# Kernel tuning notes

Measured on AMD Instinct MI355X. Metric: run time of the kernel, lower is better.

Reference implementation:

```python
import jax, jax.numpy as jnp
import numpy as np

MODES = 64        # lowest-frequency modes (mode_select_method='')
IN_CH = 512       # in_channels = H * E = 8 * 64
OUT_CH = 512      # out_channels


def setup_inputs() -> dict:
    key = jax.random.key(0)
    ks = jax.random.split(key, 5)
    B, Lq, Lkv, H, E = 32, 1024, 1024, 8, 64
    q = jax.random.normal(ks[0], (B, Lq, H, E), jnp.float32)
    k = jax.random.normal(ks[1], (B, Lkv, H, E), jnp.float32)
    v = jax.random.normal(ks[2], (B, Lkv, H, E), jnp.float32)
    scale = 1.0 / (IN_CH * OUT_CH)
    # complex weights stored as real/imag parts: [8, in//8, out//8, modes]
    Wr = scale * jax.random.uniform(ks[3], (8, IN_CH // 8, OUT_CH // 8, MODES), jnp.float32)
    Wi = scale * jax.random.uniform(ks[4], (8, IN_CH // 8, OUT_CH // 8, MODES), jnp.float32)
    return {"q": q, "k": k, "v": v, "Wr": Wr, "Wi": Wi}


def reference(q, k, v, Wr, Wi):
    # FourierCrossAttention forward (activation='tanh', lowest-mode selection).
    B, Lq, H, E = q.shape
    idx_q = jnp.arange(MODES)   # sorted lowest modes of rfft(seq_len_q)
    idx_kv = jnp.arange(MODES)  # sorted lowest modes of rfft(seq_len_kv)

    xq = jnp.transpose(q, (0, 2, 3, 1))  # [B,H,E,Lq]
    xk = jnp.transpose(k, (0, 2, 3, 1))  # [B,H,E,Lkv]

    xq_ft = jnp.fft.rfft(xq, axis=-1)[..., idx_q]    # [B,H,E,Mq] complex64
    xk_ft = jnp.fft.rfft(xk, axis=-1)[..., idx_kv]   # [B,H,E,Mkv]

    # frequency-domain attention (no conjugation, matching torch einsum)
    xqk_ft = jnp.einsum('bhex,bhey->bhxy', xq_ft, xk_ft)
    xqk_ft = jnp.tanh(xqk_ft)  # complex tanh
    xqkv_ft = jnp.einsum('bhxy,bhey->bhex', xqk_ft, xk_ft)

    W = (Wr + 1j * Wi).astype(jnp.complex64)
    xqkvw = jnp.einsum('bhex,heox->bhox', xqkv_ft, W)  # [B,H,O,Mq]

    out_ft = jnp.zeros((B, H, OUT_CH // 8, Lq // 2 + 1), jnp.complex64)
    out_ft = out_ft.at[..., idx_q].set(xqkvw)
    out = jnp.fft.irfft(out_ft / (IN_CH * OUT_CH), n=Lq, axis=-1)  # [B,H,O,Lq]
    return out
```

## Files before the change

kernel.cpp:

```cpp
#include <hip/hip_runtime.h>
#include <math.h>

#define TWO_PI_F 6.28318530717958647692f

static constexpr size_t XQR_ = 0;
static constexpr size_t XQI_ = 1048576;
static constexpr size_t XKR_ = 2097152;
static constexpr size_t XKI_ = 3145728;
static constexpr size_t TR_  = 4194304;
static constexpr size_t TI_  = 5242880;
static constexpr size_t VR_  = 6291456;
static constexpr size_t VI_  = 7340032;
static constexpr size_t WTR_ = 8388608;
static constexpr size_t WTI_ = 10485760;
static constexpr size_t UR_  = XQR_;
static constexpr size_t UI_  = XQI_;

__device__ __forceinline__ float f4c(const float4 v, int i) {
  return (i == 0) ? v.x : (i == 1) ? v.y : (i == 2) ? v.z : v.w;
}

__device__ __forceinline__ void cmac4(float4& ar, float4& ai, float sr, float si,
                                      const float4 br, const float4 bi) {
  ar.x += sr * br.x - si * bi.x;  ai.x += sr * bi.x + si * br.x;
  ar.y += sr * br.y - si * bi.y;  ai.y += sr * bi.y + si * br.y;
  ar.z += sr * br.z - si * bi.z;  ai.z += sr * bi.z + si * br.z;
  ar.w += sr * br.w - si * bi.w;  ai.w += sr * bi.w + si * br.w;
}

#define DMAC4(AR, AI, Q) \
  AR.x += Q.x * cc; AI.x -= Q.x * ss; \
  AR.y += Q.y * cc; AI.y -= Q.y * ss; \
  AR.z += Q.z * cc; AI.z -= Q.z * ss; \
  AR.w += Q.w * cc; AI.w -= Q.w * ss;

#define RMAC4(A, UR, UI) \
  A.x += cc * UR.x - ss * UI.x; \
  A.y += cc * UR.y - ss * UI.y; \
  A.z += cc * UR.z - ss * UI.z; \
  A.w += cc * UR.w - ss * UI.w;

__global__ __launch_bounds__(256) void wtrans_kernel(const float* __restrict__ Wr,
                                                     const float* __restrict__ Wi,
                                                     float* __restrict__ ws) {
  float* Wtr = ws + WTR_;
  float* Wti = ws + WTI_;
  const int h = blockIdx.x >> 6;
  const int tile = blockIdx.x & 63;
  const int t = threadIdx.x;
  __shared__ float lr[64][68], li_[64][68];
  const size_t rbase = (size_t)h * 262144 + (size_t)tile * 64 * 64;
#pragma unroll
  for (int i = 0; i < 4; ++i) {
    int idx = t + i * 256;
    int r = idx >> 4, x4 = idx & 15;
    float4 a = *(const float4*)(Wr + rbase + (size_t)r * 64 + x4 * 4);
    float4 b = *(const float4*)(Wi + rbase + (size_t)r * 64 + x4 * 4);
    *(float4*)(&lr[r][x4 * 4]) = a;
    *(float4*)(&li_[r][x4 * 4]) = b;
  }
  __syncthreads();
  const size_t wbase = (size_t)h * 262144 + (size_t)tile * 64;
#pragma unroll
  for (int i = 0; i < 4; ++i) {
    int idx = t + i * 256;
    int x = idx >> 4, r4 = idx & 15;
    float4 a, b;
    a.x = lr[r4 * 4 + 0][x]; a.y = lr[r4 * 4 + 1][x];
    a.z = lr[r4 * 4 + 2][x]; a.w = lr[r4 * 4 + 3][x];
    b.x = li_[r4 * 4 + 0][x]; b.y = li_[r4 * 4 + 1][x];
    b.z = li_[r4 * 4 + 2][x]; b.w = li_[r4 * 4 + 3][x];
    *(float4*)(Wtr + wbase + (size_t)x * 4096 + r4 * 4) = a;
    *(float4*)(Wti + wbase + (size_t)x * 4096 + r4 * 4) = b;
  }
}

__global__ __launch_bounds__(256) void dft_kernel(const float* __restrict__ q,
                                                  const float* __restrict__ k,
                                                  float* __restrict__ ws) {
  const int bi = blockIdx.x;
  const int tz = bi >> 8;
  const int b = (bi & 255) >> 3;
  const int het = bi & 7;
  const float* src = tz ? k : q;
  float* dstR = ws + (tz ? XKR_ : XQR_);
  float* dstI = ws + (tz ? XKI_ : XQI_);
  const int t = threadIdx.x;
  const int m = t & 63;
  const int heBase = (t >> 6) * 16;

  __shared__ float tile[64][64];

  float4 aR0 = {0,0,0,0}, aR1 = {0,0,0,0}, aR2 = {0,0,0,0}, aR3 = {0,0,0,0};
  float4 aI0 = {0,0,0,0}, aI1 = {0,0,0,0}, aI2 = {0,0,0,0}, aI3 = {0,0,0,0};
  float cd, sd;
  sincosf((float)m * (TWO_PI_F / 1024.0f), &sd, &cd);

  const float* srcB = src + (size_t)b * 524288 + het * 64;
  for (int c = 0; c < 16; ++c) {
    const int l0 = c * 64;
    __syncthreads();
#pragma unroll
    for (int i = 0; i < 4; ++i) {
      int idx = t + i * 256;
      int li = idx >> 4, h4 = idx & 15;
      *(float4*)(&tile[li][h4 * 4]) =
          *(const float4*)(srcB + (size_t)(l0 + li) * 512 + h4 * 4);
    }
    __syncthreads();
    int p0 = (m * l0) & 1023;
    float cc, ss;
    sincosf((float)p0 * (TWO_PI_F / 1024.0f), &ss, &cc);
#pragma unroll 4
    for (int li = 0; li < 64; ++li) {
      const float4* tr = (const float4*)(&tile[li][heBase]);
      float4 q0 = tr[0], q1 = tr[1], q2 = tr[2], q3 = tr[3];
      DMAC4(aR0, aI0, q0)
      DMAC4(aR1, aI1, q1)
      DMAC4(aR2, aI2, q2)
      DMAC4(aR3, aI3, q3)
      float nc = cc * cd - ss * sd;
      ss = cc * sd + ss * cd;
      cc = nc;
    }
  }
  float* oR = dstR + (size_t)b * 32768 + (size_t)m * 512 + het * 64 + heBase;
  float* oI = dstI + (size_t)b * 32768 + (size_t)m * 512 + het * 64 + heBase;
  ((float4*)oR)[0] = aR0; ((float4*)oR)[1] = aR1;
  ((float4*)oR)[2] = aR2; ((float4*)oR)[3] = aR3;
  ((float4*)oI)[0] = aI0; ((float4*)oI)[1] = aI1;
  ((float4*)oI)[2] = aI2; ((float4*)oI)[3] = aI3;
}

__device__ __forceinline__ void ctanh1(float a, float b, float& re, float& im) {
  float aa = fabsf(a);
  if (aa > 12.0f) {
    re = copysignf(1.0f, a);
    im = 0.0f;
    return;
  }
  float e2 = __expf(2.0f * aa);
  float ie = 1.0f / e2;
  float sh = 0.5f * (e2 - ie);
  float ch = 0.5f * (e2 + ie);
  float s2, c2;
  sincosf(2.0f * b, &s2, &c2);
  float d = ch + c2;
  float id = 1.0f / d;
  re = copysignf(sh, a) * id;
  im = s2 * id;
}

__device__ __forceinline__ void ctanh4(const float4 ar, const float4 ai, float4& tr, float4& ti) {
  ctanh1(ar.x, ai.x, tr.x, ti.x);
  ctanh1(ar.y, ai.y, tr.y, ti.y);
  ctanh1(ar.z, ai.z, tr.z, ti.z);
  ctanh1(ar.w, ai.w, tr.w, ti.w);
}

__global__ __launch_bounds__(256) void qk_tanh_kernel(float* __restrict__ ws) {
  const float* XQr = ws + XQR_;
  const float* XQi = ws + XQI_;
  const float* XKr = ws + XKR_;
  const float* XKi = ws + XKI_;
  float* Trp = ws + TR_;
  float* Tip = ws + TI_;
  const int bh = blockIdx.x;
  const int b = bh >> 3, h = bh & 7;
  const int t = threadIdx.x;
  const int x = t >> 2, yg = t & 3;
  __shared__ float Kr[64][68], Ki[64][68];
#pragma unroll
  for (int i = 0; i < 4; ++i) {
    int idx = t + i * 256;
    int yl = idx >> 4, e4 = idx & 15;
    size_t g = (size_t)b * 32768 + (size_t)yl * 512 + h * 64 + e4 * 4;
    float4 vr = *(const float4*)(XKr + g);
    float4 vi = *(const float4*)(XKi + g);
    Kr[e4 * 4 + 0][yl] = vr.x; Kr[e4 * 4 + 1][yl] = vr.y;
    Kr[e4 * 4 + 2][yl] = vr.z; Kr[e4 * 4 + 3][yl] = vr.w;
    Ki[e4 * 4 + 0][yl] = vi.x; Ki[e4 * 4 + 1][yl] = vi.y;
    Ki[e4 * 4 + 2][yl] = vi.z; Ki[e4 * 4 + 3][yl] = vi.w;
  }
  __syncthreads();
  float4 aR0 = {0,0,0,0}, aR1 = {0,0,0,0}, aR2 = {0,0,0,0}, aR3 = {0,0,0,0};
  float4 aI0 = {0,0,0,0}, aI1 = {0,0,0,0}, aI2 = {0,0,0,0}, aI3 = {0,0,0,0};
  const float* qbr = XQr + (size_t)b * 32768 + (size_t)x * 512 + h * 64;
  const float* qbi = XQi + (size_t)b * 32768 + (size_t)x * 512 + h * 64;
  for (int ec = 0; ec < 4; ++ec) {
    float4 pr[4], pim[4];
    const float4* gr = (const float4*)(qbr + ec * 16);
    const float4* gi = (const float4*)(qbi + ec * 16);
    pr[0] = gr[0]; pr[1] = gr[1]; pr[2] = gr[2]; pr[3] = gr[3];
    pim[0] = gi[0]; pim[1] = gi[1]; pim[2] = gi[2]; pim[3] = gi[3];
#pragma unroll
    for (int jj = 0; jj < 16; ++jj) {
      int e = ec * 16 + jj;
      float sr = f4c(pr[jj >> 2], jj & 3);
      float si = f4c(pim[jj >> 2], jj & 3);
      const float4* br = (const float4*)(&Kr[e][yg * 16]);
      const float4* bi = (const float4*)(&Ki[e][yg * 16]);
      cmac4(aR0, aI0, sr, si, br[0], bi[0]);
      cmac4(aR1, aI1, sr, si, br[1], bi[1]);
      cmac4(aR2, aI2, sr, si, br[2], bi[2]);
      cmac4(aR3, aI3, sr, si, br[3], bi[3]);
    }
  }
  float* oR = Trp + ((size_t)bh * 64 + x) * 64 + yg * 16;
  float* oI = Tip + ((size_t)bh * 64 + x) * 64 + yg * 16;
  float4 tR, tI;
  ctanh4(aR0, aI0, tR, tI); ((float4*)oR)[0] = tR; ((float4*)oI)[0] = tI;
  ctanh4(aR1, aI1, tR, tI); ((float4*)oR)[1] = tR; ((float4*)oI)[1] = tI;
  ctanh4(aR2, aI2, tR, tI); ((float4*)oR)[2] = tR; ((float4*)oI)[2] = tI;
  ctanh4(aR3, aI3, tR, tI); ((float4*)oR)[3] = tR; ((float4*)oI)[3] = tI;
}

__global__ __launch_bounds__(256) void xqkv_kernel(float* __restrict__ ws) {
  const float* XKr = ws + XKR_;
  const float* XKi = ws + XKI_;
  const float* Trp = ws + TR_;
  const float* Tip = ws + TI_;
  float* Vr = ws + VR_;
  float* Vi = ws + VI_;
  const int bh = blockIdx.x;
  const int b = bh >> 3, h = bh & 7;
  const int t = threadIdx.x;
  const int x = t >> 2, eg = t & 3;
  __shared__ float Kr[64][64], Ki[64][64];
#pragma unroll
  for (int i = 0; i < 4; ++i) {
    int idx = t + i * 256;
    int yl = idx >> 4, e4 = idx & 15;
    size_t g = (size_t)b * 32768 + (size_t)yl * 512 + h * 64 + e4 * 4;
    *(float4*)(&Kr[yl][e4 * 4]) = *(const float4*)(XKr + g);
    *(float4*)(&Ki[yl][e4 * 4]) = *(const float4*)(XKi + g);
  }
  __syncthreads();
  float4 aR0 = {0,0,0,0}, aR1 = {0,0,0,0}, aR2 = {0,0,0,0}, aR3 = {0,0,0,0};
  float4 aI0 = {0,0,0,0}, aI1 = {0,0,0,0}, aI2 = {0,0,0,0}, aI3 = {0,0,0,0};
  const float* tbr = Trp + ((size_t)bh * 64 + x) * 64;
  const float* tbi = Tip + ((size_t)bh * 64 + x) * 64;
  for (int yc = 0; yc < 4; ++yc) {
    float4 pr[4], pim[4];
    const float4* gr = (const float4*)(tbr + yc * 16);
    const float4* gi = (const float4*)(tbi + yc * 16);
    pr[0] = gr[0]; pr[1] = gr[1]; pr[2] = gr[2]; pr[3] = gr[3];
    pim[0] = gi[0]; pim[1] = gi[1]; pim[2] = gi[2]; pim[3] = gi[3];
#pragma unroll
    for (int jj = 0; jj < 16; ++jj) {
      int y = yc * 16 + jj;
      float sr = f4c(pr[jj >> 2], jj & 3);
      float si = f4c(pim[jj >> 2], jj & 3);
      const float4* br = (const float4*)(&Kr[y][eg * 16]);
      const float4* bi = (const float4*)(&Ki[y][eg * 16]);
      cmac4(aR0, aI0, sr, si, br[0], bi[0]);
      cmac4(aR1, aI1, sr, si, br[1], bi[1]);
      cmac4(aR2, aI2, sr, si, br[2], bi[2]);
      cmac4(aR3, aI3, sr, si, br[3], bi[3]);
    }
  }
  float* oR = Vr + ((size_t)bh * 64 + x) * 64 + eg * 16;
  float* oI = Vi + ((size_t)bh * 64 + x) * 64 + eg * 16;
  ((float4*)oR)[0] = aR0; ((float4*)oR)[1] = aR1;
  ((float4*)oR)[2] = aR2; ((float4*)oR)[3] = aR3;
  ((float4*)oI)[0] = aI0; ((float4*)oI)[1] = aI1;
  ((float4*)oI)[2] = aI2; ((float4*)oI)[3] = aI3;
}

__global__ __launch_bounds__(256) void wmul_kernel(float* __restrict__ ws) {
  const float* Vr = ws + VR_;
  const float* Vi = ws + VI_;
  float* Ur = ws + UR_;
  float* Ui = ws + UI_;
  const float* Wtr = ws + WTR_;
  const float* Wti = ws + WTI_;
  const int h = blockIdx.x >> 6, x = blockIdx.x & 63;
  const int t = threadIdx.x;
  const int bI = t >> 3, og = t & 7;
  __shared__ float Ws_r[64][64], Ws_i[64][64];
  const size_t wb = ((size_t)h * 64 + x) * 4096;
#pragma unroll
  for (int i = 0; i < 4; ++i) {
    int idx = t + i * 256;
    int el = idx >> 4, o4 = idx & 15;
    *(float4*)(&Ws_r[el][o4 * 4]) = *(const float4*)(Wtr + wb + (size_t)el * 64 + o4 * 4);
    *(float4*)(&Ws_i[el][o4 * 4]) = *(const float4*)(Wti + wb + (size_t)el * 64 + o4 * 4);
  }
  __syncthreads();
  float4 aR0 = {0,0,0,0}, aR1 = {0,0,0,0}, aI0 = {0,0,0,0}, aI1 = {0,0,0,0};
  const float* vbr = Vr + (((size_t)bI * 8 + h) * 64 + x) * 64;
  const float* vbi = Vi + (((size_t)bI * 8 + h) * 64 + x) * 64;
  for (int ec = 0; ec < 4; ++ec) {
    float4 pr[4], pim[4];
    const float4* gr = (const float4*)(vbr + ec * 16);
    const float4* gi = (const float4*)(vbi + ec * 16);
    pr[0] = gr[0]; pr[1] = gr[1]; pr[2] = gr[2]; pr[3] = gr[3];
    pim[0] = gi[0]; pim[1] = gi[1]; pim[2] = gi[2]; pim[3] = gi[3];
#pragma unroll
    for (int jj = 0; jj < 16; ++jj) {
      int e = ec * 16 + jj;
      float sr = f4c(pr[jj >> 2], jj & 3);
      float si = f4c(pim[jj >> 2], jj & 3);
      const float4* br = (const float4*)(&Ws_r[e][og * 8]);
      const float4* bi = (const float4*)(&Ws_i[e][og * 8]);
      cmac4(aR0, aI0, sr, si, br[0], bi[0]);
      cmac4(aR1, aI1, sr, si, br[1], bi[1]);
    }
  }
  float* oR = Ur + (((size_t)bI * 8 + h) * 64 + x) * 64 + og * 8;
  float* oI = Ui + (((size_t)bI * 8 + h) * 64 + x) * 64 + og * 8;
  ((float4*)oR)[0] = aR0; ((float4*)oR)[1] = aR1;
  ((float4*)oI)[0] = aI0; ((float4*)oI)[1] = aI1;
}

__global__ __launch_bounds__(256) void idft_kernel(const float* __restrict__ ws,
                                                   float* __restrict__ out) {
  const float* Ur = ws + UR_;
  const float* Ui = ws + UI_;
  const int bh = blockIdx.x >> 4;
  const int lt = blockIdx.x & 15;
  const int t = threadIdx.x;
  const int l = lt * 64 + (t & 63);
  const int og = t >> 6;
  __shared__ float Us_r[64][64], Us_i[64][64];
#pragma unroll
  for (int i = 0; i < 4; ++i) {
    int idx = t + i * 256;
    int ml = idx >> 4, o4 = idx & 15;
    size_t g = ((size_t)bh * 64 + ml) * 64 + o4 * 4;
    *(float4*)(&Us_r[ml][o4 * 4]) = *(const float4*)(Ur + g);
    *(float4*)(&Us_i[ml][o4 * 4]) = *(const float4*)(Ui + g);
  }
  __syncthreads();
  const float4* u0 = (const float4*)(&Us_r[0][og * 16]);
  float4 a0 = u0[0], a1 = u0[1], a2 = u0[2], a3 = u0[3];
  a0.x *= 0.5f; a0.y *= 0.5f; a0.z *= 0.5f; a0.w *= 0.5f;
  a1.x *= 0.5f; a1.y *= 0.5f; a1.z *= 0.5f; a1.w *= 0.5f;
  a2.x *= 0.5f; a2.y *= 0.5f; a2.z *= 0.5f; a2.w *= 0.5f;
  a3.x *= 0.5f; a3.y *= 0.5f; a3.z *= 0.5f; a3.w *= 0.5f;
  float cd, sd;
  sincosf((float)l * (TWO_PI_F / 1024.0f), &sd, &cd);
  float cc = cd, ss = sd;
#pragma unroll 4
  for (int m = 1; m < 64; ++m) {
    const float4* ur = (const float4*)(&Us_r[m][og * 16]);
    const float4* ui = (const float4*)(&Us_i[m][og * 16]);
    float4 r0 = ur[0], r1 = ur[1], r2 = ur[2], r3 = ur[3];
    float4 i0 = ui[0], i1 = ui[1], i2 = ui[2], i3 = ui[3];
    RMAC4(a0, r0, i0)
    RMAC4(a1, r1, i1)
    RMAC4(a2, r2, i2)
    RMAC4(a3, r3, i3)
    float nc = cc * cd - ss * sd;
    ss = cc * sd + ss * cd;
    cc = nc;
  }
  const float SCALE = 7.4505805969238281e-9f;
  float* ob = out + ((size_t)bh * 64 + og * 16) * 1024 + l;
  ob[0 * 1024] = a0.x * SCALE;  ob[1 * 1024] = a0.y * SCALE;
  ob[2 * 1024] = a0.z * SCALE;  ob[3 * 1024] = a0.w * SCALE;
  ob[4 * 1024] = a1.x * SCALE;  ob[5 * 1024] = a1.y * SCALE;
  ob[6 * 1024] = a1.z * SCALE;  ob[7 * 1024] = a1.w * SCALE;
  ob[8 * 1024] = a2.x * SCALE;  ob[9 * 1024] = a2.y * SCALE;
  ob[10 * 1024] = a2.z * SCALE; ob[11 * 1024] = a2.w * SCALE;
  ob[12 * 1024] = a3.x * SCALE; ob[13 * 1024] = a3.y * SCALE;
  ob[14 * 1024] = a3.z * SCALE; ob[15 * 1024] = a3.w * SCALE;
}

extern "C" void kernel_launch(void* const* d_in, const int* in_sizes, int n_in,
                              void* d_out, int out_size, void* d_ws, size_t ws_size,
                              hipStream_t stream) {
  (void)in_sizes; (void)n_in; (void)out_size; (void)ws_size;
  const float* q  = (const float*)d_in[0];
  const float* k  = (const float*)d_in[1];
  const float* Wr = (const float*)d_in[3];
  const float* Wi = (const float*)d_in[4];
  float* out = (float*)d_out;
  float* ws  = (float*)d_ws;

  hipLaunchKernelGGL(wtrans_kernel, dim3(512), dim3(256), 0, stream, Wr, Wi, ws);
  hipLaunchKernelGGL(dft_kernel,    dim3(512), dim3(256), 0, stream, q, k, ws);
  hipLaunchKernelGGL(qk_tanh_kernel,dim3(256), dim3(256), 0, stream, ws);
  hipLaunchKernelGGL(xqkv_kernel,   dim3(256), dim3(256), 0, stream, ws);
  hipLaunchKernelGGL(wmul_kernel,   dim3(512), dim3(256), 0, stream, ws);
  hipLaunchKernelGGL(idft_kernel,   dim3(4096), dim3(256), 0, stream, ws, out);
}
```

Baseline: 421.8 us.

## Rewrite DFT and QK stages in double precision with symmetric folding and retiled kernels

```diff
diff --git a/kernel.cpp b/kernel.cpp
--- a/kernel.cpp
+++ b/kernel.cpp
@@ -1,20 +1,23 @@
 #include <hip/hip_runtime.h>
 #include <math.h>
 
+
+#define TWO_PI_D 6.283185307179586476925286766559
 #define TWO_PI_F 6.28318530717958647692f
 
-static constexpr size_t XQR_ = 0;
-static constexpr size_t XQI_ = 1048576;
-static constexpr size_t XKR_ = 2097152;
-static constexpr size_t XKI_ = 3145728;
-static constexpr size_t TR_  = 4194304;
-static constexpr size_t TI_  = 5242880;
-static constexpr size_t VR_  = 6291456;
-static constexpr size_t VI_  = 7340032;
-static constexpr size_t WTR_ = 8388608;
-static constexpr size_t WTI_ = 10485760;
-static constexpr size_t UR_  = XQR_;
-static constexpr size_t UI_  = XQI_;
+static constexpr size_t MB_ = 1024 * 1024;
+static constexpr size_t XQ64R = 0;
+static constexpr size_t XQ64I = 8 * MB_;
+static constexpr size_t XK64R = 16 * MB_;
+static constexpr size_t XK64I = 24 * MB_;
+static constexpr size_t WTRb  = 0;
+static constexpr size_t WTIb  = 8 * MB_;
+static constexpr size_t TRb   = 32 * MB_;
+static constexpr size_t TIb   = 36 * MB_;
+static constexpr size_t VRb   = 40 * MB_;
+static constexpr size_t VIb   = 44 * MB_;
+static constexpr size_t URb   = 16 * MB_;
+static constexpr size_t UIb   = 20 * MB_;
 
 __device__ __forceinline__ float f4c(const float4 v, int i) {
   return (i == 0) ? v.x : (i == 1) ? v.y : (i == 2) ? v.z : v.w;
@@ -28,23 +31,11 @@
   ar.w += sr * br.w - si * bi.w;  ai.w += sr * bi.w + si * br.w;
 }
 
-#define DMAC4(AR, AI, Q) \
-  AR.x += Q.x * cc; AI.x -= Q.x * ss; \
-  AR.y += Q.y * cc; AI.y -= Q.y * ss; \
-  AR.z += Q.z * cc; AI.z -= Q.z * ss; \
-  AR.w += Q.w * cc; AI.w -= Q.w * ss;
-
-#define RMAC4(A, UR, UI) \
-  A.x += cc * UR.x - ss * UI.x; \
-  A.y += cc * UR.y - ss * UI.y; \
-  A.z += cc * UR.z - ss * UI.z; \
-  A.w += cc * UR.w - ss * UI.w;
-
 __global__ __launch_bounds__(256) void wtrans_kernel(const float* __restrict__ Wr,
                                                      const float* __restrict__ Wi,
-                                                     float* __restrict__ ws) {
-  float* Wtr = ws + WTR_;
-  float* Wti = ws + WTI_;
+                                                     char* __restrict__ wsb) {
+  float* Wtr = (float*)(wsb + WTRb);
+  float* Wti = (float*)(wsb + WTIb);
   const int h = blockIdx.x >> 6;
   const int tile = blockIdx.x & 63;
   const int t = threadIdx.x;
@@ -75,169 +66,208 @@
   }
 }
 
-__global__ __launch_bounds__(256) void dft_kernel(const float* __restrict__ q,
-                                                  const float* __restrict__ k,
-                                                  float* __restrict__ ws) {
+__global__ __launch_bounds__(128) void dft64_kernel(const float* __restrict__ q,
+                                                    const float* __restrict__ k,
+                                                    char* __restrict__ wsb) {
   const int bi = blockIdx.x;
-  const int tz = bi >> 8;
-  const int b = (bi & 255) >> 3;
-  const int het = bi & 7;
+  const int tz = bi >> 9;
+  const int b  = (bi >> 4) & 31;
+  const int het = bi & 15;
   const float* src = tz ? k : q;
-  float* dstR = ws + (tz ? XKR_ : XQR_);
-  float* dstI = ws + (tz ? XKI_ : XQI_);
-  const int t = threadIdx.x;
-  const int m = t & 63;
-  const int heBase = (t >> 6) * 16;
-
-  __shared__ float tile[64][64];
-
-  float4 aR0 = {0,0,0,0}, aR1 = {0,0,0,0}, aR2 = {0,0,0,0}, aR3 = {0,0,0,0};
-  float4 aI0 = {0,0,0,0}, aI1 = {0,0,0,0}, aI2 = {0,0,0,0}, aI3 = {0,0,0,0};
-  float cd, sd;
-  sincosf((float)m * (TWO_PI_F / 1024.0f), &sd, &cd);
-
-  const float* srcB = src + (size_t)b * 524288 + het * 64;
+  double* dR = (double*)(wsb + (tz ? XK64R : XQ64R));
+  double* dI = (double*)(wsb + (tz ? XK64I : XQ64I));
+  const int t = threadIdx.x;
+  const int mt = t & 31;
+  const int heg = t >> 5;
+  const int heL = heg * 8;
+  const int heG = het * 32;
+
+  __shared__ double sA[32][34], dA[32][34];
+
+  double re[2][8], im[2][8];
+  const float* srcB = src + (size_t)b * 524288 + heG;
+#pragma unroll
+  for (int kk = 0; kk < 8; ++kk) {
+    double x0 = (double)srcB[heL + kk];
+    double x5 = (double)srcB[262144 + heL + kk];
+    double ev = (mt & 1) ? (x0 - x5) : (x0 + x5);
+    re[0][kk] = ev; re[1][kk] = ev;
+    im[0][kk] = 0.0; im[1][kk] = 0.0;
+  }
+  double cc[2], ss[2], cd[2], sd[2];
+#pragma unroll
+  for (int mi = 0; mi < 2; ++mi) {
+    double ang = (double)(mt + mi * 32) * (TWO_PI_D / 1024.0);
+    sincos(ang, &sd[mi], &cd[mi]);
+    cc[mi] = cd[mi]; ss[mi] = sd[mi];
+  }
+  const int jrow = t >> 2, part = t & 3;
   for (int c = 0; c < 16; ++c) {
-    const int l0 = c * 64;
     __syncthreads();
-#pragma unroll
-    for (int i = 0; i < 4; ++i) {
-      int idx = t + i * 256;
-      int li = idx >> 4, h4 = idx & 15;
-      *(float4*)(&tile[li][h4 * 4]) =
-          *(const float4*)(srcB + (size_t)(l0 + li) * 512 + h4 * 4);
+    {
+      int l = c * 32 + jrow + 1;
+      const float* fw = srcB + (size_t)l * 512 + part * 8;
+      const float* mw = srcB + (size_t)(1024 - l) * 512 + part * 8;
+      float4 f0 = *(const float4*)(fw);
+      float4 f1 = *(const float4*)(fw + 4);
+      float4 m0 = *(const float4*)(mw);
+      float4 m1 = *(const float4*)(mw + 4);
+      double fv[8] = {f0.x, f0.y, f0.z, f0.w, f1.x, f1.y, f1.z, f1.w};
+      double mv[8] = {m0.x, m0.y, m0.z, m0.w, m1.x, m1.y, m1.z, m1.w};
+      if (l == 512) {
+#pragma unroll
+        for (int kk = 0; kk < 8; ++kk) { fv[kk] = 0.0; mv[kk] = 0.0; }
+      }
+#pragma unroll
+      for (int kk = 0; kk < 8; ++kk) {
+        sA[jrow][part * 8 + kk] = fv[kk] + mv[kk];
+        dA[jrow][part * 8 + kk] = fv[kk] - mv[kk];
+      }
     }
     __syncthreads();
-    int p0 = (m * l0) & 1023;
-    float cc, ss;
-    sincosf((float)p0 * (TWO_PI_F / 1024.0f), &ss, &cc);
 #pragma unroll 4
-    for (int li = 0; li < 64; ++li) {
-      const float4* tr = (const float4*)(&tile[li][heBase]);
-      float4 q0 = tr[0], q1 = tr[1], q2 = tr[2], q3 = tr[3];
-      DMAC4(aR0, aI0, q0)
-      DMAC4(aR1, aI1, q1)
-      DMAC4(aR2, aI2, q2)
-      DMAC4(aR3, aI3, q3)
-      float nc = cc * cd - ss * sd;
-      ss = cc * sd + ss * cd;
-      cc = nc;
-    }
-  }
-  float* oR = dstR + (size_t)b * 32768 + (size_t)m * 512 + het * 64 + heBase;
-  float* oI = dstI + (size_t)b * 32768 + (size_t)m * 512 + het * 64 + heBase;
-  ((float4*)oR)[0] = aR0; ((float4*)oR)[1] = aR1;
-  ((float4*)oR)[2] = aR2; ((float4*)oR)[3] = aR3;
-  ((float4*)oI)[0] = aI0; ((float4*)oI)[1] = aI1;
-  ((float4*)oI)[2] = aI2; ((float4*)oI)[3] = aI3;
-}
-
-__device__ __forceinline__ void ctanh1(float a, float b, float& re, float& im) {
-  float aa = fabsf(a);
-  if (aa > 12.0f) {
-    re = copysignf(1.0f, a);
+    for (int j = 0; j < 32; ++j) {
+      double sv[8], dv[8];
+#pragma unroll
+      for (int kk = 0; kk < 8; ++kk) { sv[kk] = sA[j][heL + kk]; dv[kk] = dA[j][heL + kk]; }
+#pragma unroll
+      for (int mi = 0; mi < 2; ++mi) {
+#pragma unroll
+        for (int kk = 0; kk < 8; ++kk) {
+          re[mi][kk] = fma(sv[kk], cc[mi], re[mi][kk]);
+          im[mi][kk] = fma(-dv[kk], ss[mi], im[mi][kk]);
+        }
+        double nc = cc[mi] * cd[mi] - ss[mi] * sd[mi];
+        ss[mi] = cc[mi] * sd[mi] + ss[mi] * cd[mi];
+        cc[mi] = nc;
+      }
+    }
+  }
+#pragma unroll
+  for (int mi = 0; mi < 2; ++mi) {
+    int m = mt + mi * 32;
+    double* oR = dR + (size_t)b * 32768 + (size_t)m * 512 + heG + heL;
+    double* oI = dI + (size_t)b * 32768 + (size_t)m * 512 + heG + heL;
+#pragma unroll
+    for (int kk = 0; kk < 8; ++kk) { oR[kk] = re[mi][kk]; oI[kk] = im[mi][kk]; }
+  }
+}
+
+__device__ __forceinline__ void ctanh_d(double a, double b, float& re, float& im) {
+  double aa = fabs(a);
+  if (aa > 12.0) {
+    re = (a >= 0.0) ? 1.0f : -1.0f;
     im = 0.0f;
     return;
   }
-  float e2 = __expf(2.0f * aa);
+  float e2 = __expf((float)(2.0 * aa));
   float ie = 1.0f / e2;
   float sh = 0.5f * (e2 - ie);
   float ch = 0.5f * (e2 + ie);
+  double phi = 2.0 * b;
+  double n = rint(phi * (1.0 / TWO_PI_D));
+  float r = (float)fma(-n, TWO_PI_D, phi);
   float s2, c2;
-  sincosf(2.0f * b, &s2, &c2);
+  sincosf(r, &s2, &c2);
   float d = ch + c2;
   float id = 1.0f / d;
-  re = copysignf(sh, a) * id;
+  re = ((a >= 0.0) ? sh : -sh) * id;
   im = s2 * id;
 }
 
-__device__ __forceinline__ void ctanh4(const float4 ar, const float4 ai, float4& tr, float4& ti) {
-  ctanh1(ar.x, ai.x, tr.x, ti.x);
-  ctanh1(ar.y, ai.y, tr.y, ti.y);
-  ctanh1(ar.z, ai.z, tr.z, ti.z);
-  ctanh1(ar.w, ai.w, tr.w, ti.w);
-}
-
-__global__ __launch_bounds__(256) void qk_tanh_kernel(float* __restrict__ ws) {
-  const float* XQr = ws + XQR_;
-  const float* XQi = ws + XQI_;
-  const float* XKr = ws + XKR_;
-  const float* XKi = ws + XKI_;
-  float* Trp = ws + TR_;
-  float* Tip = ws + TI_;
+__global__ __launch_bounds__(256) void qk_tanh_kernel(char* __restrict__ wsb) {
+  const double* Qr = (const double*)(wsb + XQ64R);
+  const double* Qi = (const double*)(wsb + XQ64I);
+  const double* Kr = (const double*)(wsb + XK64R);
+  const double* Ki = (const double*)(wsb + XK64I);
+  float* Trp = (float*)(wsb + TRb);
+  float* Tip = (float*)(wsb + TIb);
   const int bh = blockIdx.x;
   const int b = bh >> 3, h = bh & 7;
   const int t = threadIdx.x;
-  const int x = t >> 2, yg = t & 3;
-  __shared__ float Kr[64][68], Ki[64][68];
+  const int tx = t & 15, ty = t >> 4;
+  __shared__ double Qsr[16][66], Qsi[16][66], Ksr[16][66], Ksi[16][66];
+  double are[4][4] = {}, aim[4][4] = {};
+  const int row = t >> 2, ep = t & 3;
+  for (int ec = 0; ec < 4; ++ec) {
+    __syncthreads();
+    {
+      size_t g = (size_t)b * 32768 + (size_t)row * 512 + h * 64 + ec * 16 + ep * 4;
+      double2 a0, a1;
+      a0 = *(const double2*)(Qr + g); a1 = *(const double2*)(Qr + g + 2);
+      Qsr[ep*4+0][row] = a0.x; Qsr[ep*4+1][row] = a0.y;
+      Qsr[ep*4+2][row] = a1.x; Qsr[ep*4+3][row] = a1.y;
+      a0 = *(const double2*)(Qi + g); a1 = *(const double2*)(Qi + g + 2);
+      Qsi[ep*4+0][row] = a0.x; Qsi[ep*4+1][row] = a0.y;
+      Qsi[ep*4+2][row] = a1.x; Qsi[ep*4+3][row] = a1.y;
+      a0 = *(const double2*)(Kr + g); a1 = *(const double2*)(Kr + g + 2);
+      Ksr[ep*4+0][row] = a0.x; Ksr[ep*4+1][row] = a0.y;
+      Ksr[ep*4+2][row] = a1.x; Ksr[ep*4+3][row] = a1.y;
+      a0 = *(const double2*)(Ki + g); a1 = *(const double2*)(Ki + g + 2);
+      Ksi[ep*4+0][row] = a0.x; Ksi[ep*4+1][row] = a0.y;
+      Ksi[ep*4+2][row] = a1.x; Ksi[ep*4+3][row] = a1.y;
+    }
+    __syncthreads();
+#pragma unroll 4
+    for (int el = 0; el < 16; ++el) {
+      double qr[4], qi2[4], kr[4], ki2[4];
+#pragma unroll
+      for (int u = 0; u < 4; ++u) {
+        qr[u]  = Qsr[el][tx * 4 + u];
+        qi2[u] = Qsi[el][tx * 4 + u];
+        kr[u]  = Ksr[el][ty * 4 + u];
+        ki2[u] = Ksi[el][ty * 4 + u];
+      }
+#pragma unroll
+      for (int xx = 0; xx < 4; ++xx)
+#pragma unroll
+        for (int yy = 0; yy < 4; ++yy) {
+          are[xx][yy] = fma(qr[xx], kr[yy], fma(-qi2[xx], ki2[yy], are[xx][yy]));
+          aim[xx][yy] = fma(qr[xx], ki2[yy], fma(qi2[xx], kr[yy], aim[xx][yy]));
+        }
+    }
+  }
+#pragma unroll
+  for (int xx = 0; xx < 4; ++xx) {
+    int x = tx * 4 + xx;
+    float4 tR, tI;
+    ctanh_d(are[xx][0], aim[xx][0], tR.x, tI.x);
+    ctanh_d(are[xx][1], aim[xx][1], tR.y, tI.y);
+    ctanh_d(are[xx][2], aim[xx][2], tR.z, tI.z);
+    ctanh_d(are[xx][3], aim[xx][3], tR.w, tI.w);
+    *(float4*)(Trp + ((size_t)bh * 64 + x) * 64 + ty * 4) = tR;
+    *(float4*)(Tip + ((size_t)bh * 64 + x) * 64 + ty * 4) = tI;
+  }
+}
+
+__global__ __launch_bounds__(256) void xqkv_kernel(char* __restrict__ wsb) {
+  const double* XKr64 = (const double*)(wsb + XK64R);
+  const double* XKi64 = (const double*)(wsb + XK64I);
+  const float* Trp = (const float*)(wsb + TRb);
+  const float* Tip = (const float*)(wsb + TIb);
+  float* Vr = (float*)(wsb + VRb);
+  float* Vi = (float*)(wsb + VIb);
+  const int bh = blockIdx.x >> 2;
+  const int xt = blockIdx.x & 3;
+  const int b = bh >> 3, h = bh & 7;
+  const int t = threadIdx.x;
+  const int x = xt * 16 + (t >> 4);
+  const int eg = t & 15;
+  __shared__ float Kr[64][64], Ki[64][64];
 #pragma unroll
   for (int i = 0; i < 4; ++i) {
     int idx = t + i * 256;
     int yl = idx >> 4, e4 = idx & 15;
     size_t g = (size_t)b * 32768 + (size_t)yl * 512 + h * 64 + e4 * 4;
-    float4 vr = *(const float4*)(XKr + g);
-    float4 vi = *(const float4*)(XKi + g);
-    Kr[e4 * 4 + 0][yl] = vr.x; Kr[e4 * 4 + 1][yl] = vr.y;
-    Kr[e4 * 4 + 2][yl] = vr.z; Kr[e4 * 4 + 3][yl] = vr.w;
-    Ki[e4 * 4 + 0][yl] = vi.x; Ki[e4 * 4 + 1][yl] = vi.y;
-    Ki[e4 * 4 + 2][yl] = vi.z; Ki[e4 * 4 + 3][yl] = vi.w;
+    double2 r0 = *(const double2*)(XKr64 + g);
+    double2 r1 = *(const double2*)(XKr64 + g + 2);
+    double2 i0 = *(const double2*)(XKi64 + g);
+    double2 i1 = *(const double2*)(XKi64 + g + 2);
+    *(float4*)(&Kr[yl][e4 * 4]) = make_float4((float)r0.x, (float)r0.y, (float)r1.x, (float)r1.y);
+    *(float4*)(&Ki[yl][e4 * 4]) = make_float4((float)i0.x, (float)i0.y, (float)i1.x, (float)i1.y);
   }
   __syncthreads();
-  float4 aR0 = {0,0,0,0}, aR1 = {0,0,0,0}, aR2 = {0,0,0,0}, aR3 = {0,0,0,0};
-  float4 aI0 = {0,0,0,0}, aI1 = {0,0,0,0}, aI2 = {0,0,0,0}, aI3 = {0,0,0,0};
-  const float* qbr = XQr + (size_t)b * 32768 + (size_t)x * 512 + h * 64;
-  const float* qbi = XQi + (size_t)b * 32768 + (size_t)x * 512 + h * 64;
-  for (int ec = 0; ec < 4; ++ec) {
-    float4 pr[4], pim[4];
-    const float4* gr = (const float4*)(qbr + ec * 16);
-    const float4* gi = (const float4*)(qbi + ec * 16);
-    pr[0] = gr[0]; pr[1] = gr[1]; pr[2] = gr[2]; pr[3] = gr[3];
-    pim[0] = gi[0]; pim[1] = gi[1]; pim[2] = gi[2]; pim[3] = gi[3];
-#pragma unroll
-    for (int jj = 0; jj < 16; ++jj) {
-      int e = ec * 16 + jj;
-      float sr = f4c(pr[jj >> 2], jj & 3);
-      float si = f4c(pim[jj >> 2], jj & 3);
-      const float4* br = (const float4*)(&Kr[e][yg * 16]);
-      const float4* bi = (const float4*)(&Ki[e][yg * 16]);
-      cmac4(aR0, aI0, sr, si, br[0], bi[0]);
-      cmac4(aR1, aI1, sr, si, br[1], bi[1]);
-      cmac4(aR2, aI2, sr, si, br[2], bi[2]);
-      cmac4(aR3, aI3, sr, si, br[3], bi[3]);
-    }
-  }
-  float* oR = Trp + ((size_t)bh * 64 + x) * 64 + yg * 16;
-  float* oI = Tip + ((size_t)bh * 64 + x) * 64 + yg * 16;
-  float4 tR, tI;
-  ctanh4(aR0, aI0, tR, tI); ((float4*)oR)[0] = tR; ((float4*)oI)[0] = tI;
-  ctanh4(aR1, aI1, tR, tI); ((float4*)oR)[1] = tR; ((float4*)oI)[1] = tI;
-  ctanh4(aR2, aI2, tR, tI); ((float4*)oR)[2] = tR; ((float4*)oI)[2] = tI;
-  ctanh4(aR3, aI3, tR, tI); ((float4*)oR)[3] = tR; ((float4*)oI)[3] = tI;
-}
-
-__global__ __launch_bounds__(256) void xqkv_kernel(float* __restrict__ ws) {
-  const float* XKr = ws + XKR_;
-  const float* XKi = ws + XKI_;
-  const float* Trp = ws + TR_;
-  const float* Tip = ws + TI_;
-  float* Vr = ws + VR_;
-  float* Vi = ws + VI_;
-  const int bh = blockIdx.x;
-  const int b = bh >> 3, h = bh & 7;
-  const int t = threadIdx.x;
-  const int x = t >> 2, eg = t & 3;
-  __shared__ float Kr[64][64], Ki[64][64];
-#pragma unroll
-  for (int i = 0; i < 4; ++i) {
-    int idx = t + i * 256;
-    int yl = idx >> 4, e4 = idx & 15;
-    size_t g = (size_t)b * 32768 + (size_t)yl * 512 + h * 64 + e4 * 4;
-    *(float4*)(&Kr[yl][e4 * 4]) = *(const float4*)(XKr + g);
-    *(float4*)(&Ki[yl][e4 * 4]) = *(const float4*)(XKi + g);
-  }
-  __syncthreads();
-  float4 aR0 = {0,0,0,0}, aR1 = {0,0,0,0}, aR2 = {0,0,0,0}, aR3 = {0,0,0,0};
-  float4 aI0 = {0,0,0,0}, aI1 = {0,0,0,0}, aI2 = {0,0,0,0}, aI3 = {0,0,0,0};
+  float4 aR = {0,0,0,0}, aI = {0,0,0,0};
   const float* tbr = Trp + ((size_t)bh * 64 + x) * 64;
   const float* tbi = Tip + ((size_t)bh * 64 + x) * 64;
   for (int yc = 0; yc < 4; ++yc) {
@@ -251,32 +281,30 @@
       int y = yc * 16 + jj;
       float sr = f4c(pr[jj >> 2], jj & 3);
       float si = f4c(pim[jj >> 2], jj & 3);
-      const float4* br = (const float4*)(&Kr[y][eg * 16]);
-      const float4* bi = (const float4*)(&Ki[y][eg * 16]);
-      cmac4(aR0, aI0, sr, si, br[0], bi[0]);
-      cmac4(aR1, aI1, sr, si, br[1], bi[1]);
-      cmac4(aR2, aI2, sr, si, br[2], bi[2]);
-      cmac4(aR3, aI3, sr, si, br[3], bi[3]);
-    }
-  }
-  float* oR = Vr + ((size_t)bh * 64 + x) * 64 + eg * 16;
-  float* oI = Vi + ((size_t)bh * 64 + x) * 64 + eg * 16;
-  ((float4*)oR)[0] = aR0; ((float4*)oR)[1] = aR1;
-  ((float4*)oR)[2] = aR2; ((float4*)oR)[3] = aR3;
-  ((float4*)oI)[0] = aI0; ((float4*)oI)[1] = aI1;
-  ((float4*)oI)[2] = aI2; ((float4*)oI)[3] = aI3;
-}
-
-__global__ __launch_bounds__(256) void wmul_kernel(float* __restrict__ ws) {
-  const float* Vr = ws + VR_;
-  const float* Vi = ws + VI_;
-  float* Ur = ws + UR_;
-  float* Ui = ws + UI_;
-  const float* Wtr = ws + WTR_;
-  const float* Wti = ws + WTI_;
-  const int h = blockIdx.x >> 6, x = blockIdx.x & 63;
-  const int t = threadIdx.x;
-  const int bI = t >> 3, og = t & 7;
+      const float4 br = *(const float4*)(&Kr[y][eg * 4]);
+      const float4 bi = *(const float4*)(&Ki[y][eg * 4]);
+      cmac4(aR, aI, sr, si, br, bi);
+    }
+  }
+  float* oR = Vr + ((size_t)bh * 64 + x) * 64 + eg * 4;
+  float* oI = Vi + ((size_t)bh * 64 + x) * 64 + eg * 4;
+  *(float4*)oR = aR;
+  *(float4*)oI = aI;
+}
+
+__global__ __launch_bounds__(256) void wmul_kernel(char* __restrict__ wsb) {
+  const float* Vr = (const float*)(wsb + VRb);
+  const float* Vi = (const float*)(wsb + VIb);
+  float* Ur = (float*)(wsb + URb);
+  float* Ui = (float*)(wsb + UIb);
+  const float* Wtr = (const float*)(wsb + WTRb);
+  const float* Wti = (const float*)(wsb + WTIb);
+  const int h = blockIdx.x >> 7;
+  const int x = (blockIdx.x >> 1) & 63;
+  const int bt = blockIdx.x & 1;
+  const int t = threadIdx.x;
+  const int bI = bt * 16 + (t >> 4);
+  const int og = t & 15;
   __shared__ float Ws_r[64][64], Ws_i[64][64];
   const size_t wb = ((size_t)h * 64 + x) * 4096;
 #pragma unroll
@@ -287,7 +315,7 @@
     *(float4*)(&Ws_i[el][o4 * 4]) = *(const float4*)(Wti + wb + (size_t)el * 64 + o4 * 4);
   }
   __syncthreads();
-  float4 aR0 = {0,0,0,0}, aR1 = {0,0,0,0}, aI0 = {0,0,0,0}, aI1 = {0,0,0,0};
+  float4 aR = {0,0,0,0}, aI = {0,0,0,0};
   const float* vbr = Vr + (((size_t)bI * 8 + h) * 64 + x) * 64;
   const float* vbi = Vi + (((size_t)bI * 8 + h) * 64 + x) * 64;
   for (int ec = 0; ec < 4; ++ec) {
@@ -301,24 +329,23 @@
       int e = ec * 16 + jj;
       float sr = f4c(pr[jj >> 2], jj & 3);
       float si = f4c(pim[jj >> 2], jj & 3);
-      const float4* br = (const float4*)(&Ws_r[e][og * 8]);
-      const float4* bi = (const float4*)(&Ws_i[e][og * 8]);
-      cmac4(aR0, aI0, sr, si, br[0], bi[0]);
-      cmac4(aR1, aI1, sr, si, br[1], bi[1]);
-    }
-  }
-  float* oR = Ur + (((size_t)bI * 8 + h) * 64 + x) * 64 + og * 8;
-  float* oI = Ui + (((size_t)bI * 8 + h) * 64 + x) * 64 + og * 8;
-  ((float4*)oR)[0] = aR0; ((float4*)oR)[1] = aR1;
-  ((float4*)oI)[0] = aI0; ((float4*)oI)[1] = aI1;
-}
-
-__global__ __launch_bounds__(256) void idft_kernel(const float* __restrict__ ws,
+      const float4 br = *(const float4*)(&Ws_r[e][og * 4]);
+      const float4 bi = *(const float4*)(&Ws_i[e][og * 4]);
+      cmac4(aR, aI, sr, si, br, bi);
+    }
+  }
+  float* oR = Ur + (((size_t)bI * 8 + h) * 64 + x) * 64 + og * 4;
+  float* oI = Ui + (((size_t)bI * 8 + h) * 64 + x) * 64 + og * 4;
+  *(float4*)oR = aR;
+  *(float4*)oI = aI;
+}
+
+__global__ __launch_bounds__(256) void idft_kernel(const char* __restrict__ wsb,
                                                    float* __restrict__ out) {
-  const float* Ur = ws + UR_;
-  const float* Ui = ws + UI_;
-  const int bh = blockIdx.x >> 4;
-  const int lt = blockIdx.x & 15;
+  const float* Ur = (const float*)(wsb + URb);
+  const float* Ui = (const float*)(wsb + UIb);
+  const int bh = blockIdx.x >> 2;
+  const int lt = blockIdx.x & 3;
   const int t = threadIdx.x;
   const int l = lt * 64 + (t & 63);
   const int og = t >> 6;
@@ -332,12 +359,14 @@
     *(float4*)(&Us_i[ml][o4 * 4]) = *(const float4*)(Ui + g);
   }
   __syncthreads();
+  float4 a[4][4];
   const float4* u0 = (const float4*)(&Us_r[0][og * 16]);
-  float4 a0 = u0[0], a1 = u0[1], a2 = u0[2], a3 = u0[3];
-  a0.x *= 0.5f; a0.y *= 0.5f; a0.z *= 0.5f; a0.w *= 0.5f;
-  a1.x *= 0.5f; a1.y *= 0.5f; a1.z *= 0.5f; a1.w *= 0.5f;
-  a2.x *= 0.5f; a2.y *= 0.5f; a2.z *= 0.5f; a2.w *= 0.5f;
-  a3.x *= 0.5f; a3.y *= 0.5f; a3.z *= 0.5f; a3.w *= 0.5f;
+#pragma unroll
+  for (int j = 0; j < 4; ++j) {
+    float4 v = u0[j];
+    v.x *= 0.5f; v.y *= 0.5f; v.z *= 0.5f; v.w *= 0.5f;
+    a[0][j] = v; a[1][j] = v; a[2][j] = v; a[3][j] = v;
+  }
   float cd, sd;
   sincosf((float)l * (TWO_PI_F / 1024.0f), &sd, &cd);
   float cc = cd, ss = sd;
@@ -345,26 +374,36 @@
   for (int m = 1; m < 64; ++m) {
     const float4* ur = (const float4*)(&Us_r[m][og * 16]);
     const float4* ui = (const float4*)(&Us_i[m][og * 16]);
-    float4 r0 = ur[0], r1 = ur[1], r2 = ur[2], r3 = ur[3];
-    float4 i0 = ui[0], i1 = ui[1], i2 = ui[2], i3 = ui[3];
-    RMAC4(a0, r0, i0)
-    RMAC4(a1, r1, i1)
-    RMAC4(a2, r2, i2)
-    RMAC4(a3, r3, i3)
+    float4 R[4], I[4];
+#pragma unroll
+    for (int j = 0; j < 4; ++j) { R[j] = ur[j]; I[j] = ui[j]; }
+#pragma unroll
+    for (int k = 0; k < 4; ++k) {
+      int rot = (m * k) & 3;
+      float cP = (rot == 0) ? cc : (rot == 1) ? -ss : (rot == 2) ? -cc : ss;
+      float sP = (rot == 0) ? ss : (rot == 1) ? cc : (rot == 2) ? -ss : -cc;
+#pragma unroll
+      for (int j = 0; j < 4; ++j) {
+        a[k][j].x += cP * R[j].x - sP * I[j].x;
+        a[k][j].y += cP * R[j].y - sP * I[j].y;
+        a[k][j].z += cP * R[j].z - sP * I[j].z;
+        a[k][j].w += cP * R[j].w - sP * I[j].w;
+      }
+    }
     float nc = cc * cd - ss * sd;
     ss = cc * sd + ss * cd;
     cc = nc;
   }
   const float SCALE = 7.4505805969238281e-9f;
-  float* ob = out + ((size_t)bh * 64 + og * 16) * 1024 + l;
-  ob[0 * 1024] = a0.x * SCALE;  ob[1 * 1024] = a0.y * SCALE;
-  ob[2 * 1024] = a0.z * SCALE;  ob[3 * 1024] = a0.w * SCALE;
-  ob[4 * 1024] = a1.x * SCALE;  ob[5 * 1024] = a1.y * SCALE;
-  ob[6 * 1024] = a1.z * SCALE;  ob[7 * 1024] = a1.w * SCALE;
-  ob[8 * 1024] = a2.x * SCALE;  ob[9 * 1024] = a2.y * SCALE;
-  ob[10 * 1024] = a2.z * SCALE; ob[11 * 1024] = a2.w * SCALE;
-  ob[12 * 1024] = a3.x * SCALE; ob[13 * 1024] = a3.y * SCALE;
-  ob[14 * 1024] = a3.z * SCALE; ob[15 * 1024] = a3.w * SCALE;
+  float* obase = out + ((size_t)bh * 64 + og * 16) * 1024 + l;
+#pragma unroll
+  for (int k = 0; k < 4; ++k) {
+    float* ob = obase + 256 * k;
+#pragma unroll
+    for (int r = 0; r < 16; ++r) {
+      ob[(size_t)r * 1024] = f4c(a[k][r >> 2], r & 3) * SCALE;
+    }
+  }
 }
 
 extern "C" void kernel_launch(void* const* d_in, const int* in_sizes, int n_in,
@@ -376,12 +415,12 @@
   const float* Wr = (const float*)d_in[3];
   const float* Wi = (const float*)d_in[4];
   float* out = (float*)d_out;
-  float* ws  = (float*)d_ws;
-
-  hipLaunchKernelGGL(wtrans_kernel, dim3(512), dim3(256), 0, stream, Wr, Wi, ws);
-  hipLaunchKernelGGL(dft_kernel,    dim3(512), dim3(256), 0, stream, q, k, ws);
-  hipLaunchKernelGGL(qk_tanh_kernel,dim3(256), dim3(256), 0, stream, ws);
-  hipLaunchKernelGGL(xqkv_kernel,   dim3(256), dim3(256), 0, stream, ws);
-  hipLaunchKernelGGL(wmul_kernel,   dim3(512), dim3(256), 0, stream, ws);
-  hipLaunchKernelGGL(idft_kernel,   dim3(4096), dim3(256), 0, stream, ws, out);
-}
+  char* wsb  = (char*)d_ws;
+
+  hipLaunchKernelGGL(dft64_kernel,   dim3(1024), dim3(128), 0, stream, q, k, wsb);
+  hipLaunchKernelGGL(qk_tanh_kernel, dim3(256),  dim3(256), 0, stream, wsb);
+  hipLaunchKernelGGL(wtrans_kernel,  dim3(512),  dim3(256), 0, stream, Wr, Wi, wsb);
+  hipLaunchKernelGGL(xqkv_kernel,    dim3(1024), dim3(256), 0, stream, wsb);
+  hipLaunchKernelGGL(wmul_kernel,    dim3(1024), dim3(256), 0, stream, wsb);
+  hipLaunchKernelGGL(idft_kernel,    dim3(1024), dim3(256), 0, stream, wsb, out);
+}
```

Result: faster. 410.9 us (-2.6%).
